# Performance work log

Hardware: AMD Instinct MI355X
Metric: run time of the kernel (lower is better)

## Reference

```python
import jax, jax.numpy as jnp
import numpy as np

N = 100000      # num nodes
E = 1600000     # num edges (avg degree 16)
F_IN = 700      # hardcoded in_feats in build()
H = 128         # args.hidden
EPS = 1e-5      # BatchNorm1d eps


def setup_inputs() -> dict:
    key = jax.random.key(0)
    ks = jax.random.split(key, 12)
    w = lambda k, shape: jax.random.normal(k, shape, dtype=jnp.float32) * 0.05
    return {
        "inputs": jax.random.normal(ks[0], (1, N, F_IN), dtype=jnp.float32),
        "graph": jax.random.randint(ks[1], (1, E, 2), 0, N, dtype=jnp.int32),
        "Wself0": w(ks[2], (F_IN, H)),
        "Wneigh0": w(ks[3], (F_IN, H)),
        "b0": jnp.zeros((H,), jnp.float32),
        "Wself": w(ks[4], (3, H, H)),
        "Wneigh": w(ks[5], (3, H, H)),
        "b": jnp.zeros((3, H), jnp.float32),
        "bn_gamma": jnp.ones((4, H), jnp.float32),
        "bn_beta": jnp.zeros((4, H), jnp.float32),
        "W1": w(ks[6], (H, 64)),
        "b1": jnp.zeros((64,), jnp.float32),
        "bng1": jnp.ones((64,), jnp.float32),
        "bnb1": jnp.zeros((64,), jnp.float32),
        "W2": w(ks[7], (64, 1)),
        "b2": jnp.zeros((1,), jnp.float32),
    }


def _batch_norm(x, g, beta):
    # training-mode BN over node dim (biased variance, as PyTorch normalizes)
    mu = jnp.mean(x, axis=0)
    var = jnp.mean((x - mu) ** 2, axis=0)
    return (x - mu) * jax.lax.rsqrt(var + EPS) * g + beta


def reference(inputs, graph, Wself0, Wneigh0, b0, Wself, Wneigh, b,
              bn_gamma, bn_beta, W1, b1, bng1, bnb1, W2, b2):
    h = inputs[0]                      # [N, F_IN] (squeeze + flatten is a no-op)
    edges = graph[0]                   # [E, 2]
    src, dst = edges[:, 0], edges[:, 1]
    deg = jax.ops.segment_sum(jnp.ones((E,), jnp.float32), dst, num_segments=N)
    denom = jnp.maximum(deg, 1.0)[:, None]   # DGL clamps zero in-degree

    def sage(x, Ws, Wn, bias):
        # SAGEConv(mean): fc before message passing (linearity => equivalent)
        hn = x @ Wn                                                   # [N, H]
        agg = jax.ops.segment_sum(hn[src], dst, num_segments=N) / denom
        return x @ Ws + agg + bias

    # layer 0: no residual
    h = sage(h, Wself0, Wneigh0, b0)
    h = jax.nn.relu(_batch_norm(h, bn_gamma[0], bn_beta[0]))
    # layers 1..3: BN + residual + relu (dropout = identity in eval)
    for l in range(3):
        pre = h
        h = sage(h, Wself[l], Wneigh[l], b[l])
        h = _batch_norm(h, bn_gamma[l + 1], bn_beta[l + 1])
        h = jax.nn.relu(h + pre)

    z = _batch_norm(h @ W1 + b1, bng1, bnb1)
    z = jax.nn.relu(z)
    out = z @ W2 + b2                  # [N, 1]
    return out.T                       # permute(1,0) -> [1, N]
```

## Files before the change

kernel.cpp:

```cpp
#include <hip/hip_runtime.h>
#include <hip/hip_bf16.h>

#define N_NODES 100000
#define N_EDGES 1600000
#define F_IN    700
#define NKB0    22
#define HDIM    128
#define SCAN_B  256
#define NB_SCAN ((N_NODES + SCAN_B - 1) / SCAN_B)

typedef _Float16 half8 __attribute__((ext_vector_type(8)));
typedef _Float16 half4 __attribute__((ext_vector_type(4)));
typedef float floatx4 __attribute__((ext_vector_type(4)));

__device__ __forceinline__ void cp16(const void* g, void* l) {
    __builtin_amdgcn_global_load_lds(
        (const __attribute__((address_space(1))) void*)g,
        (__attribute__((address_space(3))) void*)l, 16, 0, 0);
}

__global__ void count_edges(const int* __restrict__ graph, int* __restrict__ cnt) {
    int e = blockIdx.x * blockDim.x + threadIdx.x;
    if (e < N_EDGES) atomicAdd(&cnt[graph[2 * e + 1]], 1);
}

__global__ void scan1(const int* __restrict__ cnt, int* __restrict__ incl,
                      int* __restrict__ blk) {
    __shared__ int s[SCAN_B];
    int tid = threadIdx.x;
    int i = blockIdx.x * SCAN_B + tid;
    s[tid] = (i < N_NODES) ? cnt[i] : 0;
    __syncthreads();
    for (int off = 1; off < SCAN_B; off <<= 1) {
        int t = (tid >= off) ? s[tid - off] : 0;
        __syncthreads();
        s[tid] += t;
        __syncthreads();
    }
    if (i < N_NODES) incl[i] = s[tid];
    if (tid == SCAN_B - 1) blk[blockIdx.x] = s[tid];
}

__global__ void scan2(const int* __restrict__ blk, int* __restrict__ blkoff) {
    __shared__ int s[512];
    int tid = threadIdx.x;
    s[tid] = (tid < NB_SCAN) ? blk[tid] : 0;
    __syncthreads();
    for (int off = 1; off < 512; off <<= 1) {
        int t = (tid >= off) ? s[tid - off] : 0;
        __syncthreads();
        s[tid] += t;
        __syncthreads();
    }
    if (tid < NB_SCAN) blkoff[tid] = (tid == 0) ? 0 : s[tid - 1];
}

__global__ void scan3(const int* __restrict__ incl, const int* __restrict__ blkoff,
                      int* __restrict__ row_ptr) {
    int i = blockIdx.x * SCAN_B + threadIdx.x;
    if (i < N_NODES) {
        row_ptr[i + 1] = incl[i] + blkoff[i >> 8];
        if (i == 0) row_ptr[0] = 0;
    }
}

__global__ void fill_edges(const int* __restrict__ graph, const int* __restrict__ row_ptr,
                           int* __restrict__ cursor, int* __restrict__ esrc) {
    int e = blockIdx.x * blockDim.x + threadIdx.x;
    if (e < N_EDGES) {
        int src = graph[2 * e];
        int dst = graph[2 * e + 1];
        esrc[row_ptr[dst] + atomicAdd(&cursor[dst], 1)] = src;
    }
}

__global__ void build_wtp0(const float* __restrict__ Wn, const float* __restrict__ Ws,
                           _Float16* __restrict__ out) {
    int q = blockIdx.x * blockDim.x + threadIdx.x;
    if (q >= NKB0 * 256 * 4) return;
    int kb = q >> 10;
    int r  = (q >> 2) & 255;
    int cc = q & 3;
    int k0 = kb * 32 + (cc ^ ((r >> 1) & 3)) * 8;
    half8 v;
    #pragma unroll
    for (int e = 0; e < 8; e++) {
        int k = k0 + e;
        float f = 0.0f;
        if (k < F_IN) f = (r < 128) ? Wn[k * 128 + r] : Ws[k * 128 + (r - 128)];
        v[e] = (_Float16)f;
    }
    *(half8*)&out[(size_t)q * 8] = v;
}

__global__ void build_wtpl(const float* __restrict__ Wn, const float* __restrict__ Ws,
                           _Float16* __restrict__ out) {
    int q = blockIdx.x * blockDim.x + threadIdx.x;
    if (q >= 3 * 4 * 256 * 4) return;
    int l = q >> 12;
    int rem = q & 4095;
    int kb = rem >> 10;
    int r  = (rem >> 2) & 255;
    int cc = rem & 3;
    int k0 = kb * 32 + (cc ^ ((r >> 1) & 3)) * 8;
    half8 v;
    #pragma unroll
    for (int e = 0; e < 8; e++) {
        int k = k0 + e;
        float f = (r < 128) ? Wn[l * 16384 + k * 128 + r]
                            : Ws[l * 16384 + k * 128 + (r - 128)];
        v[e] = (_Float16)f;
    }
    *(half8*)&out[(size_t)q * 8] = v;
}

__global__ __launch_bounds__(256) void gemm0_ns(
    const float* __restrict__ A, int M, int K,
    const _Float16* __restrict__ Wtp, const float* __restrict__ bias,
    const float* __restrict__ zbuf,
    _Float16* __restrict__ Cn, float* __restrict__ Cs) {
    __shared__ char sbuf[2][24576];

    int tid = threadIdx.x;
    int wave = tid >> 6, lane = tid & 63;
    int lm = lane & 15, quad = lane >> 4;
    int wm = wave >> 1, wn = wave & 1;
    int bx = blockIdx.x;
    long row0 = (long)(bx >> 1) * 128;
    int nh = bx & 1;

    floatx4 acc[4][4] = {};

    auto stage = [&](int kb, char* buf) {
        #pragma unroll
        for (int pass = 0; pass < 4; pass++) {
            int q = pass * 256 + tid;
            int r = q >> 3, cc = q & 7;
            int ccg = cc ^ (r & 7);
            long grow = row0 + r;
            if (grow >= M) grow = 0;
            int gk = kb * 32 + ccg * 4;
            const float* src = (gk + 4 <= K) ? (A + grow * (long)K + gk) : zbuf;
            cp16(src, buf + pass * 4096 + wave * 1024);
        }
        const _Float16* wsrc = Wtp + (size_t)kb * 8192 + nh * 4096;
        #pragma unroll
        for (int pass = 0; pass < 2; pass++) {
            cp16(wsrc + (size_t)(pass * 256 + tid) * 8,
                 buf + 16384 + pass * 4096 + wave * 1024);
        }
    };

    stage(0, sbuf[0]);

    for (int kb = 0; kb < NKB0; kb++) {
        int p = kb & 1;
        if (kb + 1 < NKB0) {
            stage(kb + 1, sbuf[p ^ 1]);
            asm volatile("s_waitcnt vmcnt(6)\n\ts_barrier" ::: "memory");
        } else {
            asm volatile("s_waitcnt vmcnt(0)\n\ts_barrier" ::: "memory");
        }

        const float* Af = (const float*)sbuf[p];
        const _Float16* Bf = (const _Float16*)(sbuf[p] + 16384);
        half8 af[4];
        #pragma unroll
        for (int i = 0; i < 4; i++) {
            int row = wm * 64 + i * 16 + lm;
            int c0 = (quad * 2) ^ (row & 7);
            int c1 = (quad * 2 + 1) ^ (row & 7);
            floatx4 f0 = *(const floatx4*)&Af[row * 32 + c0 * 4];
            floatx4 f1 = *(const floatx4*)&Af[row * 32 + c1 * 4];
            af[i][0] = (_Float16)f0[0]; af[i][1] = (_Float16)f0[1];
            af[i][2] = (_Float16)f0[2]; af[i][3] = (_Float16)f0[3];
            af[i][4] = (_Float16)f1[0]; af[i][5] = (_Float16)f1[1];
            af[i][6] = (_Float16)f1[2]; af[i][7] = (_Float16)f1[3];
        }
        #pragma unroll
        for (int j = 0; j < 4; j++) {
            int brow = wn * 64 + j * 16 + lm;
            int ch = quad ^ ((brow >> 1) & 3);
            half8 bf = *(const half8*)&Bf[brow * 32 + ch * 8];
            #pragma unroll
            for (int i = 0; i < 4; i++)
                acc[i][j] = __builtin_amdgcn_mfma_f32_16x16x32_f16(af[i], bf, acc[i][j], 0, 0, 0);
        }
        asm volatile("s_waitcnt lgkmcnt(0)\n\ts_barrier" ::: "memory");
    }

    #pragma unroll
    for (int i = 0; i < 4; i++) {
        long r0 = row0 + wm * 64 + i * 16 + quad * 4;
        #pragma unroll
        for (int j = 0; j < 4; j++) {
            int c = wn * 64 + j * 16 + lm;
            if (nh) {
                float badd = bias[c];
                #pragma unroll
                for (int rr = 0; rr < 4; rr++) {
                    long r = r0 + rr;
                    if (r < M) Cs[r * HDIM + c] = acc[i][j][rr] + badd;
                }
            } else {
                #pragma unroll
                for (int rr = 0; rr < 4; rr++) {
                    long r = r0 + rr;
                    if (r < M) Cn[r * HDIM + c] = (_Float16)acc[i][j][rr];
                }
            }
        }
    }
}

__global__ __launch_bounds__(256) void gemm16_ns(
    const _Float16* __restrict__ A, int M,
    const _Float16* __restrict__ Wtp, const float* __restrict__ bias,
    _Float16* __restrict__ Cn, float* __restrict__ Cs) {
    __shared__ _Float16 sbuf[2][8192];

    int tid = threadIdx.x;
    int wave = tid >> 6, lane = tid & 63;
    int lm = lane & 15, quad = lane >> 4;
    int wm = wave >> 1, wn = wave & 1;
    int bx = blockIdx.x;
    long row0 = (long)(bx >> 1) * 128;
    int nh = bx & 1;

    floatx4 acc[4][4] = {};

    auto stage = [&](int kb, _Float16* buf) {
        #pragma unroll
        for (int pass = 0; pass < 2; pass++) {
            int q = pass * 256 + tid;
            int r = q >> 2, cc = q & 3;
            int ccg = cc ^ ((r >> 1) & 3);
            long grow = row0 + r;
            if (grow >= M) grow = 0;
            cp16(A + grow * (long)HDIM + kb * 32 + ccg * 8,
                 buf + pass * 2048 + wave * 512);
        }
        const _Float16* wsrc = Wtp + (size_t)kb * 8192 + nh * 4096;
        #pragma unroll
        for (int pass = 0; pass < 2; pass++) {
            cp16(wsrc + (size_t)(pass * 256 + tid) * 8,
                 buf + 4096 + pass * 2048 + wave * 512);
        }
    };

    stage(0, sbuf[0]);

    for (int kb = 0; kb < 4; kb++) {
        int p = kb & 1;
        if (kb + 1 < 4) {
            stage(kb + 1, sbuf[p ^ 1]);
            asm volatile("s_waitcnt vmcnt(4)\n\ts_barrier" ::: "memory");
        } else {
            asm volatile("s_waitcnt vmcnt(0)\n\ts_barrier" ::: "memory");
        }

        const _Float16* bp = sbuf[p];
        half8 af[4];
        #pragma unroll
        for (int i = 0; i < 4; i++) {
            int row = wm * 64 + i * 16 + lm;
            int ch = quad ^ ((row >> 1) & 3);
            af[i] = *(const half8*)&bp[row * 32 + ch * 8];
        }
        #pragma unroll
        for (int j = 0; j < 4; j++) {
            int brow = wn * 64 + j * 16 + lm;
            int ch = quad ^ ((brow >> 1) & 3);
            half8 bf = *(const half8*)&bp[4096 + brow * 32 + ch * 8];
            #pragma unroll
            for (int i = 0; i < 4; i++)
                acc[i][j] = __builtin_amdgcn_mfma_f32_16x16x32_f16(af[i], bf, acc[i][j], 0, 0, 0);
        }
        asm volatile("s_waitcnt lgkmcnt(0)\n\ts_barrier" ::: "memory");
    }

    #pragma unroll
    for (int i = 0; i < 4; i++) {
        long r0 = row0 + wm * 64 + i * 16 + quad * 4;
        #pragma unroll
        for (int j = 0; j < 4; j++) {
            int c = wn * 64 + j * 16 + lm;
            if (nh) {
                float badd = bias[c];
                #pragma unroll
                for (int rr = 0; rr < 4; rr++) {
                    long r = r0 + rr;
                    if (r < M) Cs[r * HDIM + c] = acc[i][j][rr] + badd;
                }
            } else {
                #pragma unroll
                for (int rr = 0; rr < 4; rr++) {
                    long r = r0 + rr;
                    if (r < M) Cn[r * HDIM + c] = (_Float16)acc[i][j][rr];
                }
            }
        }
    }
}

__global__ __launch_bounds__(256) void aggregate_w(
    const _Float16* __restrict__ hn, const int* __restrict__ row_ptr,
    const int* __restrict__ esrc, float* __restrict__ pre) {
    int wave = threadIdx.x >> 6, lane = threadIdx.x & 63;
    int n = blockIdx.x * 4 + wave;
    if (n >= N_NODES) return;
    int start = row_ptr[n], end = row_ptr[n + 1];
    int eg = lane >> 4;
    int c8 = (lane & 15) * 8;

    float acc[8] = {};
    for (int base = start; base < end; base += 16) {
        #pragma unroll
        for (int u = 0; u < 4; u++) {
            int e = base + u * 4 + eg;
            if (e < end) {
                int s = esrc[e];
                half8 v = *(const half8*)&hn[(size_t)s * HDIM + c8];
                #pragma unroll
                for (int i = 0; i < 8; i++) acc[i] += (float)v[i];
            }
        }
    }
    #pragma unroll
    for (int i = 0; i < 8; i++) {
        acc[i] += __shfl_xor(acc[i], 16, 64);
        acc[i] += __shfl_xor(acc[i], 32, 64);
    }
    if (eg == 0) {
        float rd = 1.0f / (float)max(end - start, 1);
        size_t off = (size_t)n * HDIM + c8;
        float4 p0 = *(float4*)&pre[off];
        float4 p1 = *(float4*)&pre[off + 4];
        p0.x += acc[0] * rd; p0.y += acc[1] * rd;
        p0.z += acc[2] * rd; p0.w += acc[3] * rd;
        p1.x += acc[4] * rd; p1.y += acc[5] * rd;
        p1.z += acc[6] * rd; p1.w += acc[7] * rd;
        *(float4*)&pre[off]     = p0;
        *(float4*)&pre[off + 4] = p1;
    }
}

__global__ void bn_stats(const float* __restrict__ P, float* __restrict__ gsum,
                         float* __restrict__ gsumsq, int M, int C) {
    int tid = threadIdx.x;
    int c = tid % C;
    int rpb = 256 / C;
    float s = 0.0f, s2 = 0.0f;
    for (int r = blockIdx.x * rpb + tid / C; r < M; r += gridDim.x * rpb) {
        float v = P[(size_t)r * C + c];
        s += v; s2 += v * v;
    }
    __shared__ float ss[256], ss2[256];
    ss[tid] = s; ss2[tid] = s2;
    __syncthreads();
    for (int off = 128; off >= C; off >>= 1) {
        if (tid < off) { ss[tid] += ss[tid + off]; ss2[tid] += ss2[tid + off]; }
        __syncthreads();
    }
    if (tid < C) {
        atomicAdd(&gsum[tid], ss[tid]);
        atomicAdd(&gsumsq[tid], ss2[tid]);
    }
}

__global__ void bn_apply16(const float* __restrict__ P, const _Float16* __restrict__ res16,
                           _Float16* __restrict__ out16,
                           const float* __restrict__ gsum, const float* __restrict__ gsumsq,
                           const float* __restrict__ gamma, const float* __restrict__ beta,
                           int M, int total4, int Cdiv4) {
    __shared__ float ssc[HDIM], ssh[HDIM];
    int tid = threadIdx.x;
    int C = Cdiv4 * 4;
    if (tid < C) {
        float mean = gsum[tid] / (float)M;
        float var = gsumsq[tid] / (float)M - mean * mean;
        float sc = rsqrtf(var + 1e-5f) * gamma[tid];
        ssc[tid] = sc;
        ssh[tid] = beta[tid] - mean * sc;
    }
    __syncthreads();
    for (int f = blockIdx.x * blockDim.x + tid; f < total4;
         f += gridDim.x * blockDim.x) {
        int c4 = (f % Cdiv4) * 4;
        float4 v = ((const float4*)P)[f];
        v.x = v.x * ssc[c4 + 0] + ssh[c4 + 0];
        v.y = v.y * ssc[c4 + 1] + ssh[c4 + 1];
        v.z = v.z * ssc[c4 + 2] + ssh[c4 + 2];
        v.w = v.w * ssc[c4 + 3] + ssh[c4 + 3];
        if (res16) {
            half4 rv = *(const half4*)&res16[(size_t)f * 4];
            v.x += (float)rv[0]; v.y += (float)rv[1];
            v.z += (float)rv[2]; v.w += (float)rv[3];
        }
        half4 h;
        h[0] = (_Float16)fmaxf(v.x, 0.0f); h[1] = (_Float16)fmaxf(v.y, 0.0f);
        h[2] = (_Float16)fmaxf(v.z, 0.0f); h[3] = (_Float16)fmaxf(v.w, 0.0f);
        *(half4*)&out16[(size_t)f * 4] = h;
    }
}

__global__ __launch_bounds__(256) void mlp_gemm(const _Float16* __restrict__ H,
                                                const float* __restrict__ W1,
                                                const float* __restrict__ b1,
                                                float* __restrict__ Z, int M) {
    __shared__ float hs[64 * 132];
    __shared__ float ws[128 * 64];
    int tid = threadIdx.x;
    int tx = tid & 15;
    int ty = tid >> 4;
    int row0 = blockIdx.x * 64;

    #pragma unroll
    for (int t = 0; t < 8; t++) {
        int f = tid + t * 256;
        int r = f >> 4, c4 = (f & 15) * 4;
        *(float4*)&ws[r * 64 + c4] = *(const float4*)&W1[r * 64 + c4];
    }
    #pragma unroll
    for (int t = 0; t < 4; t++) {
        int f = tid + t * 256;
        int r = f >> 4, c8 = (f & 15) * 8;
        int gr = row0 + r;
        if (gr < M) {
            half8 hv = *(const half8*)&H[(size_t)gr * HDIM + c8];
            #pragma unroll
            for (int i = 0; i < 8; i++) hs[r * 132 + c8 + i] = (float)hv[i];
        } else {
            #pragma unroll
            for (int i = 0; i < 8; i++) hs[r * 132 + c8 + i] = 0.0f;
        }
    }
    __syncthreads();

    float acc[4][4] = {};
    for (int k = 0; k < 128; k++) {
        float a[4];
        #pragma unroll
        for (int i = 0; i < 4; i++) a[i] = hs[(ty * 4 + i) * 132 + k];
        float4 b4 = *(const float4*)&ws[k * 64 + tx * 4];
        #pragma unroll
        for (int i = 0; i < 4; i++) {
            acc[i][0] += a[i] * b4.x; acc[i][1] += a[i] * b4.y;
            acc[i][2] += a[i] * b4.z; acc[i][3] += a[i] * b4.w;
        }
    }
    float4 bb = *(const float4*)&b1[tx * 4];
    #pragma unroll
    for (int i = 0; i < 4; i++) {
        int r = row0 + ty * 4 + i;
        if (r < M) {
            float4 v = {acc[i][0] + bb.x, acc[i][1] + bb.y,
                        acc[i][2] + bb.z, acc[i][3] + bb.w};
            *(float4*)&Z[(size_t)r * 64 + tx * 4] = v;
        }
    }
}

__global__ void final_out(const float* __restrict__ Z,
                          const float* __restrict__ gsum, const float* __restrict__ gsumsq,
                          const float* __restrict__ gamma, const float* __restrict__ beta,
                          const float* __restrict__ W2, const float* __restrict__ b2,
                          float* __restrict__ out, int M) {
    __shared__ float ssc[64], ssh[64], sw[64];
    int tid = threadIdx.x;
    if (tid < 64) {
        float mean = gsum[tid] / (float)M;
        float var = gsumsq[tid] / (float)M - mean * mean;
        float sc = rsqrtf(var + 1e-5f) * gamma[tid];
        ssc[tid] = sc;
        ssh[tid] = beta[tid] - mean * sc;
        sw[tid] = W2[tid];
    }
    __syncthreads();
    int n = blockIdx.x * 4 + (tid >> 6);
    int lane = tid & 63;
    if (n >= N_NODES) return;
    float z = Z[(size_t)n * 64 + lane] * ssc[lane] + ssh[lane];
    z = fmaxf(z, 0.0f);
    float v = z * sw[lane];
    #pragma unroll
    for (int off = 32; off >= 1; off >>= 1) v += __shfl_down(v, off, 64);
    if (lane == 0) out[n] = v + b2[0];
}

extern "C" void kernel_launch(void* const* d_in, const int* in_sizes, int n_in,
                              void* d_out, int out_size, void* d_ws, size_t ws_size,
                              hipStream_t stream) {
    const float* X       = (const float*)d_in[0];
    const int*   graph   = (const int*)d_in[1];
    const float* Wself0  = (const float*)d_in[2];
    const float* Wneigh0 = (const float*)d_in[3];
    const float* b0      = (const float*)d_in[4];
    const float* Wself   = (const float*)d_in[5];
    const float* Wneigh  = (const float*)d_in[6];
    const float* bvec    = (const float*)d_in[7];
    const float* bn_g    = (const float*)d_in[8];
    const float* bn_b    = (const float*)d_in[9];
    const float* W1      = (const float*)d_in[10];
    const float* b1      = (const float*)d_in[11];
    const float* bng1    = (const float*)d_in[12];
    const float* bnb1    = (const float*)d_in[13];
    const float* W2      = (const float*)d_in[14];
    const float* b2      = (const float*)d_in[15];
    float* out = (float*)d_out;

    size_t off = 0;
    auto alloc = [&](size_t bytes) {
        void* p = (char*)d_ws + off;
        off += (bytes + 255) & ~(size_t)255;
        return p;
    };
    int* cnt     = (int*)alloc(N_NODES * 4);
    int* cursor  = (int*)alloc(N_NODES * 4);
    int* row_ptr = (int*)alloc((N_NODES + 1) * 4);
    int* incl    = (int*)alloc(N_NODES * 4);
    int* blk     = (int*)alloc(NB_SCAN * 4);
    int* blkoff  = (int*)alloc(NB_SCAN * 4);
    int* esrc    = (int*)alloc((size_t)N_EDGES * 4);
    float*    pre   = (float*)alloc((size_t)N_NODES * HDIM * 4);
    _Float16* h16A  = (_Float16*)alloc((size_t)N_NODES * HDIM * 2);
    _Float16* h16B  = (_Float16*)alloc((size_t)N_NODES * HDIM * 2);
    _Float16* hn16  = (_Float16*)alloc((size_t)N_NODES * HDIM * 2);
    float*    Z     = (float*)alloc((size_t)N_NODES * 64 * 4);
    _Float16* Wtp0  = (_Float16*)alloc((size_t)NKB0 * 8192 * 2);
    _Float16* Wtpl  = (_Float16*)alloc((size_t)3 * 4 * 8192 * 2);
    float*    zbuf  = (float*)alloc(256);
    float* stats = (float*)alloc(256 * 4);
    float* gsum = stats, *gsumsq = stats + 128;

    const int EB = (N_EDGES + 255) / 256;
    const int GB = ((N_NODES + 127) / 128) * 2;
    const int AGB = (N_NODES + 3) / 4;

    hipMemsetAsync(cnt, 0, N_NODES * 4, stream);
    hipMemsetAsync(cursor, 0, N_NODES * 4, stream);
    hipMemsetAsync(zbuf, 0, 256, stream);
    count_edges<<<EB, 256, 0, stream>>>(graph, cnt);
    scan1<<<NB_SCAN, SCAN_B, 0, stream>>>(cnt, incl, blk);
    scan2<<<1, 512, 0, stream>>>(blk, blkoff);
    scan3<<<NB_SCAN, SCAN_B, 0, stream>>>(incl, blkoff, row_ptr);
    fill_edges<<<EB, 256, 0, stream>>>(graph, row_ptr, cursor, esrc);

    build_wtp0<<<(NKB0 * 1024 + 255) / 256, 256, 0, stream>>>(Wneigh0, Wself0, Wtp0);
    build_wtpl<<<(3 * 4096 + 255) / 256, 256, 0, stream>>>(Wneigh, Wself, Wtpl);

    _Float16* hc = h16A;
    _Float16* hx = h16B;

    gemm0_ns<<<GB, 256, 0, stream>>>(X, N_NODES, F_IN, Wtp0, b0, zbuf, hn16, pre);
    aggregate_w<<<AGB, 256, 0, stream>>>(hn16, row_ptr, esrc, pre);
    hipMemsetAsync(stats, 0, 256 * 4, stream);
    bn_stats<<<512, 256, 0, stream>>>(pre, gsum, gsumsq, N_NODES, 128);
    bn_apply16<<<1024, 256, 0, stream>>>(pre, nullptr, hc, gsum, gsumsq,
                                         bn_g, bn_b, N_NODES,
                                         N_NODES * HDIM / 4, HDIM / 4);

    for (int l = 0; l < 3; l++) {
        gemm16_ns<<<GB, 256, 0, stream>>>(hc, N_NODES, Wtpl + (size_t)l * 32768,
                                          bvec + l * HDIM, hn16, pre);
        aggregate_w<<<AGB, 256, 0, stream>>>(hn16, row_ptr, esrc, pre);
        hipMemsetAsync(stats, 0, 256 * 4, stream);
        bn_stats<<<512, 256, 0, stream>>>(pre, gsum, gsumsq, N_NODES, 128);
        bn_apply16<<<1024, 256, 0, stream>>>(pre, hc, hx, gsum, gsumsq,
                                             bn_g + (l + 1) * HDIM,
                                             bn_b + (l + 1) * HDIM, N_NODES,
                                             N_NODES * HDIM / 4, HDIM / 4);
        _Float16* t = hc; hc = hx; hx = t;
    }

    mlp_gemm<<<(N_NODES + 63) / 64, 256, 0, stream>>>(hc, W1, b1, Z, N_NODES);
    hipMemsetAsync(stats, 0, 256 * 4, stream);
    bn_stats<<<512, 256, 0, stream>>>(Z, gsum, gsumsq, N_NODES, 64);
    final_out<<<AGB, 256, 0, stream>>>(Z, gsum, gsumsq, bng1, bnb1, W2, b2,
                                       out, N_NODES);
}
```

Baseline: 1.333 ms.

## Stage layer-0 GEMM A tiles through registers and store fp16 in LDS

The first-layer GEMM no longer copies fp32 input tiles straight from global memory into LDS with global_load_lds. Each thread now loads its A and B fragments into registers two k-blocks ahead, converts A to fp16 once, and writes fp16 tiles into a smaller double-buffered LDS area. This removes the repeated fp32-to-fp16 conversion each wave did on LDS reads and cuts LDS use, which may allow more resident blocks. In exchange it adds register pressure and puts VGPR round-trips and LDS writes into the main loop, where the earlier asynchronous path avoided them.

```diff
diff --git a/kernel.cpp b/kernel.cpp
--- a/kernel.cpp
+++ b/kernel.cpp
@@ -17,6 +17,12 @@
     __builtin_amdgcn_global_load_lds(
         (const __attribute__((address_space(1))) void*)g,
         (__attribute__((address_space(3))) void*)l, 16, 0, 0);
+}
+
+__device__ __forceinline__ floatx4 ld4u(const float* p) {
+    floatx4 v;
+    __builtin_memcpy(&v, p, 16);
+    return v;
 }
 
 __global__ void count_edges(const int* __restrict__ graph, int* __restrict__ cnt) {
@@ -114,12 +120,12 @@
     *(half8*)&out[(size_t)q * 8] = v;
 }
 
-__global__ __launch_bounds__(256) void gemm0_ns(
+__global__ __launch_bounds__(256) void gemm0_rs(
     const float* __restrict__ A, int M, int K,
     const _Float16* __restrict__ Wtp, const float* __restrict__ bias,
     const float* __restrict__ zbuf,
     _Float16* __restrict__ Cn, float* __restrict__ Cs) {
-    __shared__ char sbuf[2][24576];
+    __shared__ _Float16 sbuf[2][8192];
 
     int tid = threadIdx.x;
     int wave = tid >> 6, lane = tid & 63;
@@ -129,64 +135,81 @@
     long row0 = (long)(bx >> 1) * 128;
     int nh = bx & 1;
 
+    int ra1 = tid >> 2, s4 = tid & 3;
+    int ra2 = 64 + ra1;
+    int cc1 = s4 ^ ((ra1 >> 1) & 3);
+    int cc2 = s4 ^ ((ra2 >> 1) & 3);
+    long ga1 = row0 + ra1; if (ga1 >= M) ga1 = 0;
+    long ga2 = row0 + ra2; if (ga2 >= M) ga2 = 0;
+    const float* arow1 = A + ga1 * (long)K;
+    const float* arow2 = A + ga2 * (long)K;
+    const _Float16* wbase = Wtp + nh * 4096;
+
+    floatx4 R[4];
+    half8 Bv[2];
+
+    auto loadA = [&](int kb) {
+        int k1 = kb * 32 + cc1 * 8;
+        int k2 = kb * 32 + cc2 * 8;
+        R[0] = (k1 + 4 <= K) ? ld4u(arow1 + k1)     : ld4u(zbuf);
+        R[1] = (k1 + 8 <= K) ? ld4u(arow1 + k1 + 4) : ld4u(zbuf);
+        R[2] = (k2 + 4 <= K) ? ld4u(arow2 + k2)     : ld4u(zbuf);
+        R[3] = (k2 + 8 <= K) ? ld4u(arow2 + k2 + 4) : ld4u(zbuf);
+    };
+    auto loadB = [&](int kb) {
+        const _Float16* wsrc = wbase + (size_t)kb * 8192;
+        Bv[0] = *(const half8*)(wsrc + tid * 8);
+        Bv[1] = *(const half8*)(wsrc + 2048 + tid * 8);
+    };
+    auto writeAB = [&](_Float16* buf) {
+        half8 h1, h2;
+        #pragma unroll
+        for (int e = 0; e < 4; e++) {
+            h1[e]     = (_Float16)R[0][e];
+            h1[e + 4] = (_Float16)R[1][e];
+            h2[e]     = (_Float16)R[2][e];
+            h2[e + 4] = (_Float16)R[3][e];
+        }
+        *(half8*)&buf[ra1 * 32 + s4 * 8] = h1;
+        *(half8*)&buf[ra2 * 32 + s4 * 8] = h2;
+        *(half8*)&buf[4096 + tid * 8]        = Bv[0];
+        *(half8*)&buf[4096 + 2048 + tid * 8] = Bv[1];
+    };
+
     floatx4 acc[4][4] = {};
 
-    auto stage = [&](int kb, char* buf) {
-        #pragma unroll
-        for (int pass = 0; pass < 4; pass++) {
-            int q = pass * 256 + tid;
-            int r = q >> 3, cc = q & 7;
-            int ccg = cc ^ (r & 7);
-            long grow = row0 + r;
-            if (grow >= M) grow = 0;
-            int gk = kb * 32 + ccg * 4;
-            const float* src = (gk + 4 <= K) ? (A + grow * (long)K + gk) : zbuf;
-            cp16(src, buf + pass * 4096 + wave * 1024);
-        }
-        const _Float16* wsrc = Wtp + (size_t)kb * 8192 + nh * 4096;
-        #pragma unroll
-        for (int pass = 0; pass < 2; pass++) {
-            cp16(wsrc + (size_t)(pass * 256 + tid) * 8,
-                 buf + 16384 + pass * 4096 + wave * 1024);
-        }
-    };
-
-    stage(0, sbuf[0]);
-
+    loadA(0); loadB(0);
+    writeAB(sbuf[0]);
+    loadA(1); loadB(1);
+    asm volatile("s_waitcnt lgkmcnt(0)\n\ts_barrier" ::: "memory");
+
+    #pragma unroll 2
     for (int kb = 0; kb < NKB0; kb++) {
         int p = kb & 1;
-        if (kb + 1 < NKB0) {
-            stage(kb + 1, sbuf[p ^ 1]);
-            asm volatile("s_waitcnt vmcnt(6)\n\ts_barrier" ::: "memory");
-        } else {
-            asm volatile("s_waitcnt vmcnt(0)\n\ts_barrier" ::: "memory");
-        }
-
-        const float* Af = (const float*)sbuf[p];
-        const _Float16* Bf = (const _Float16*)(sbuf[p] + 16384);
+        const _Float16* bp = sbuf[p];
+
         half8 af[4];
         #pragma unroll
         for (int i = 0; i < 4; i++) {
             int row = wm * 64 + i * 16 + lm;
-            int c0 = (quad * 2) ^ (row & 7);
-            int c1 = (quad * 2 + 1) ^ (row & 7);
-            floatx4 f0 = *(const floatx4*)&Af[row * 32 + c0 * 4];
-            floatx4 f1 = *(const floatx4*)&Af[row * 32 + c1 * 4];
-            af[i][0] = (_Float16)f0[0]; af[i][1] = (_Float16)f0[1];
-            af[i][2] = (_Float16)f0[2]; af[i][3] = (_Float16)f0[3];
-            af[i][4] = (_Float16)f1[0]; af[i][5] = (_Float16)f1[1];
-            af[i][6] = (_Float16)f1[2]; af[i][7] = (_Float16)f1[3];
+            int ch = quad ^ ((row >> 1) & 3);
+            af[i] = *(const half8*)&bp[row * 32 + ch * 8];
         }
         #pragma unroll
         for (int j = 0; j < 4; j++) {
             int brow = wn * 64 + j * 16 + lm;
             int ch = quad ^ ((brow >> 1) & 3);
-            half8 bf = *(const half8*)&Bf[brow * 32 + ch * 8];
+            half8 bf = *(const half8*)&bp[4096 + brow * 32 + ch * 8];
             #pragma unroll
             for (int i = 0; i < 4; i++)
                 acc[i][j] = __builtin_amdgcn_mfma_f32_16x16x32_f16(af[i], bf, acc[i][j], 0, 0, 0);
         }
-        asm volatile("s_waitcnt lgkmcnt(0)\n\ts_barrier" ::: "memory");
+
+        if (kb + 1 < NKB0) {
+            writeAB(sbuf[p ^ 1]);
+            if (kb + 2 < NKB0) { loadA(kb + 2); loadB(kb + 2); }
+            asm volatile("s_waitcnt lgkmcnt(0)\n\ts_barrier" ::: "memory");
+        }
     }
 
     #pragma unroll
@@ -552,7 +575,7 @@
     _Float16* hc = h16A;
     _Float16* hx = h16B;
 
-    gemm0_ns<<<GB, 256, 0, stream>>>(X, N_NODES, F_IN, Wtp0, b0, zbuf, hn16, pre);
+    gemm0_rs<<<GB, 256, 0, stream>>>(X, N_NODES, F_IN, Wtp0, b0, zbuf, hn16, pre);
     aggregate_w<<<AGB, 256, 0, stream>>>(hn16, row_ptr, esrc, pre);
     hipMemsetAsync(stats, 0, 256 * 4, stream);
     bn_stats<<<512, 256, 0, stream>>>(pre, gsum, gsumsq, N_NODES, 128);
```

Result: no change. 1.337 ms (+0.3%).

## Fuse BatchNorm statistics into aggregate and MLP kernels with sharded atomics

Applied to the files above, without the earlier changes.

Removes the separate bn_stats kernels by accumulating per-channel sum and sum-of-squares inside aggregate_w and mlp_gemm. Each block first reduces in shared memory, then atomically adds into one of 64 shards to limit atomic contention. The consumers (bn_apply16, final_out) sum the shards before computing mean and variance. This drops one full read pass over the pre-activation and Z buffers per layer, at the cost of a shared-memory reduction, a barrier and extra atomics in the fused kernels.

```diff
diff --git a/kernel.cpp b/kernel.cpp
--- a/kernel.cpp
+++ b/kernel.cpp
@@ -8,6 +8,7 @@
 #define HDIM    128
 #define SCAN_B  256
 #define NB_SCAN ((N_NODES + SCAN_B - 1) / SCAN_B)
+#define NSHARD  64
 
 typedef _Float16 half8 __attribute__((ext_vector_type(8)));
 typedef _Float16 half4 __attribute__((ext_vector_type(4)));
@@ -305,80 +306,87 @@
 
 __global__ __launch_bounds__(256) void aggregate_w(
     const _Float16* __restrict__ hn, const int* __restrict__ row_ptr,
-    const int* __restrict__ esrc, float* __restrict__ pre) {
-    int wave = threadIdx.x >> 6, lane = threadIdx.x & 63;
+    const int* __restrict__ esrc, float* __restrict__ pre,
+    float* __restrict__ stats) {
+    __shared__ float s1[4][HDIM], s2[4][HDIM];
+    int tid = threadIdx.x;
+    int wave = tid >> 6, lane = tid & 63;
     int n = blockIdx.x * 4 + wave;
-    if (n >= N_NODES) return;
-    int start = row_ptr[n], end = row_ptr[n + 1];
+    bool valid = (n < N_NODES);
     int eg = lane >> 4;
     int c8 = (lane & 15) * 8;
 
-    float acc[8] = {};
-    for (int base = start; base < end; base += 16) {
-        #pragma unroll
-        for (int u = 0; u < 4; u++) {
-            int e = base + u * 4 + eg;
-            if (e < end) {
-                int s = esrc[e];
-                half8 v = *(const half8*)&hn[(size_t)s * HDIM + c8];
-                #pragma unroll
-                for (int i = 0; i < 8; i++) acc[i] += (float)v[i];
+    float pv[8] = {};
+    if (valid) {
+        int start = row_ptr[n], end = row_ptr[n + 1];
+        float acc[8] = {};
+        for (int base = start; base < end; base += 16) {
+            #pragma unroll
+            for (int u = 0; u < 4; u++) {
+                int e = base + u * 4 + eg;
+                if (e < end) {
+                    int s = esrc[e];
+                    half8 v = *(const half8*)&hn[(size_t)s * HDIM + c8];
+                    #pragma unroll
+                    for (int i = 0; i < 8; i++) acc[i] += (float)v[i];
+                }
             }
         }
-    }
-    #pragma unroll
-    for (int i = 0; i < 8; i++) {
-        acc[i] += __shfl_xor(acc[i], 16, 64);
-        acc[i] += __shfl_xor(acc[i], 32, 64);
+        #pragma unroll
+        for (int i = 0; i < 8; i++) {
+            acc[i] += __shfl_xor(acc[i], 16, 64);
+            acc[i] += __shfl_xor(acc[i], 32, 64);
+        }
+        if (eg == 0) {
+            float rd = 1.0f / (float)max(end - start, 1);
+            size_t off = (size_t)n * HDIM + c8;
+            float4 p0 = *(float4*)&pre[off];
+            float4 p1 = *(float4*)&pre[off + 4];
+            p0.x += acc[0] * rd; p0.y += acc[1] * rd;
+            p0.z += acc[2] * rd; p0.w += acc[3] * rd;
+            p1.x += acc[4] * rd; p1.y += acc[5] * rd;
+            p1.z += acc[6] * rd; p1.w += acc[7] * rd;
+            *(float4*)&pre[off]     = p0;
+            *(float4*)&pre[off + 4] = p1;
+            pv[0] = p0.x; pv[1] = p0.y; pv[2] = p0.z; pv[3] = p0.w;
+            pv[4] = p1.x; pv[5] = p1.y; pv[6] = p1.z; pv[7] = p1.w;
+        }
     }
     if (eg == 0) {
-        float rd = 1.0f / (float)max(end - start, 1);
-        size_t off = (size_t)n * HDIM + c8;
-        float4 p0 = *(float4*)&pre[off];
-        float4 p1 = *(float4*)&pre[off + 4];
-        p0.x += acc[0] * rd; p0.y += acc[1] * rd;
-        p0.z += acc[2] * rd; p0.w += acc[3] * rd;
-        p1.x += acc[4] * rd; p1.y += acc[5] * rd;
-        p1.z += acc[6] * rd; p1.w += acc[7] * rd;
-        *(float4*)&pre[off]     = p0;
-        *(float4*)&pre[off + 4] = p1;
-    }
-}
-
-__global__ void bn_stats(const float* __restrict__ P, float* __restrict__ gsum,
-                         float* __restrict__ gsumsq, int M, int C) {
-    int tid = threadIdx.x;
-    int c = tid % C;
-    int rpb = 256 / C;
-    float s = 0.0f, s2 = 0.0f;
-    for (int r = blockIdx.x * rpb + tid / C; r < M; r += gridDim.x * rpb) {
-        float v = P[(size_t)r * C + c];
-        s += v; s2 += v * v;
-    }
-    __shared__ float ss[256], ss2[256];
-    ss[tid] = s; ss2[tid] = s2;
+        #pragma unroll
+        for (int i = 0; i < 8; i++) {
+            float v = valid ? pv[i] : 0.0f;
+            s1[wave][c8 + i] = v;
+            s2[wave][c8 + i] = v * v;
+        }
+    }
     __syncthreads();
-    for (int off = 128; off >= C; off >>= 1) {
-        if (tid < off) { ss[tid] += ss[tid + off]; ss2[tid] += ss2[tid + off]; }
-        __syncthreads();
-    }
-    if (tid < C) {
-        atomicAdd(&gsum[tid], ss[tid]);
-        atomicAdd(&gsumsq[tid], ss2[tid]);
+    if (tid < HDIM) {
+        float a = s1[0][tid] + s1[1][tid] + s1[2][tid] + s1[3][tid];
+        float b = s2[0][tid] + s2[1][tid] + s2[2][tid] + s2[3][tid];
+        float* sh = stats + (size_t)(blockIdx.x & (NSHARD - 1)) * 256;
+        atomicAdd(&sh[tid], a);
+        atomicAdd(&sh[128 + tid], b);
     }
 }
 
 __global__ void bn_apply16(const float* __restrict__ P, const _Float16* __restrict__ res16,
                            _Float16* __restrict__ out16,
-                           const float* __restrict__ gsum, const float* __restrict__ gsumsq,
+                           const float* __restrict__ stats,
                            const float* __restrict__ gamma, const float* __restrict__ beta,
                            int M, int total4, int Cdiv4) {
     __shared__ float ssc[HDIM], ssh[HDIM];
     int tid = threadIdx.x;
     int C = Cdiv4 * 4;
     if (tid < C) {
-        float mean = gsum[tid] / (float)M;
-        float var = gsumsq[tid] / (float)M - mean * mean;
+        float s = 0.0f, s2 = 0.0f;
+        #pragma unroll 8
+        for (int k = 0; k < NSHARD; k++) {
+            s  += stats[k * 256 + tid];
+            s2 += stats[k * 256 + 128 + tid];
+        }
+        float mean = s / (float)M;
+        float var = s2 / (float)M - mean * mean;
         float sc = rsqrtf(var + 1e-5f) * gamma[tid];
         ssc[tid] = sc;
         ssh[tid] = beta[tid] - mean * sc;
@@ -407,9 +415,11 @@
 __global__ __launch_bounds__(256) void mlp_gemm(const _Float16* __restrict__ H,
                                                 const float* __restrict__ W1,
                                                 const float* __restrict__ b1,
-                                                float* __restrict__ Z, int M) {
+                                                float* __restrict__ Z,
+                                                float* __restrict__ stats, int M) {
     __shared__ float hs[64 * 132];
     __shared__ float ws[128 * 64];
+    __shared__ float zs1[16][64], zs2[16][64];
     int tid = threadIdx.x;
     int tx = tid & 15;
     int ty = tid >> 4;
@@ -450,27 +460,55 @@
         }
     }
     float4 bb = *(const float4*)&b1[tx * 4];
+    float cs[4] = {}, cq[4] = {};
     #pragma unroll
     for (int i = 0; i < 4; i++) {
         int r = row0 + ty * 4 + i;
         if (r < M) {
-            float4 v = {acc[i][0] + bb.x, acc[i][1] + bb.y,
-                        acc[i][2] + bb.z, acc[i][3] + bb.w};
+            float v0 = acc[i][0] + bb.x;
+            float v1 = acc[i][1] + bb.y;
+            float v2 = acc[i][2] + bb.z;
+            float v3 = acc[i][3] + bb.w;
+            float4 v = {v0, v1, v2, v3};
             *(float4*)&Z[(size_t)r * 64 + tx * 4] = v;
-        }
+            cs[0] += v0; cq[0] += v0 * v0;
+            cs[1] += v1; cq[1] += v1 * v1;
+            cs[2] += v2; cq[2] += v2 * v2;
+            cs[3] += v3; cq[3] += v3 * v3;
+        }
+    }
+    #pragma unroll
+    for (int j = 0; j < 4; j++) {
+        zs1[ty][tx * 4 + j] = cs[j];
+        zs2[ty][tx * 4 + j] = cq[j];
+    }
+    __syncthreads();
+    if (tid < 64) {
+        float a = 0.0f, b = 0.0f;
+        #pragma unroll
+        for (int k = 0; k < 16; k++) { a += zs1[k][tid]; b += zs2[k][tid]; }
+        float* sh = stats + (size_t)(blockIdx.x & (NSHARD - 1)) * 256;
+        atomicAdd(&sh[tid], a);
+        atomicAdd(&sh[128 + tid], b);
     }
 }
 
 __global__ void final_out(const float* __restrict__ Z,
-                          const float* __restrict__ gsum, const float* __restrict__ gsumsq,
+                          const float* __restrict__ stats,
                           const float* __restrict__ gamma, const float* __restrict__ beta,
                           const float* __restrict__ W2, const float* __restrict__ b2,
                           float* __restrict__ out, int M) {
     __shared__ float ssc[64], ssh[64], sw[64];
     int tid = threadIdx.x;
     if (tid < 64) {
-        float mean = gsum[tid] / (float)M;
-        float var = gsumsq[tid] / (float)M - mean * mean;
+        float s = 0.0f, s2 = 0.0f;
+        #pragma unroll 8
+        for (int k = 0; k < NSHARD; k++) {
+            s  += stats[k * 256 + tid];
+            s2 += stats[k * 256 + 128 + tid];
+        }
+        float mean = s / (float)M;
+        float var = s2 / (float)M - mean * mean;
         float sc = rsqrtf(var + 1e-5f) * gamma[tid];
         ssc[tid] = sc;
         ssh[tid] = beta[tid] - mean * sc;
@@ -530,12 +568,12 @@
     _Float16* Wtp0  = (_Float16*)alloc((size_t)NKB0 * 8192 * 2);
     _Float16* Wtpl  = (_Float16*)alloc((size_t)3 * 4 * 8192 * 2);
     float*    zbuf  = (float*)alloc(256);
-    float* stats = (float*)alloc(256 * 4);
-    float* gsum = stats, *gsumsq = stats + 128;
+    float*    stats = (float*)alloc((size_t)NSHARD * 256 * 4);
 
     const int EB = (N_EDGES + 255) / 256;
     const int GB = ((N_NODES + 127) / 128) * 2;
     const int AGB = (N_NODES + 3) / 4;
+    const size_t STB = (size_t)NSHARD * 256 * 4;
 
     hipMemsetAsync(cnt, 0, N_NODES * 4, stream);
     hipMemsetAsync(cursor, 0, N_NODES * 4, stream);
@@ -553,29 +591,26 @@
     _Float16* hx = h16B;
 
     gemm0_ns<<<GB, 256, 0, stream>>>(X, N_NODES, F_IN, Wtp0, b0, zbuf, hn16, pre);
-    aggregate_w<<<AGB, 256, 0, stream>>>(hn16, row_ptr, esrc, pre);
-    hipMemsetAsync(stats, 0, 256 * 4, stream);
-    bn_stats<<<512, 256, 0, stream>>>(pre, gsum, gsumsq, N_NODES, 128);
-    bn_apply16<<<1024, 256, 0, stream>>>(pre, nullptr, hc, gsum, gsumsq,
+    hipMemsetAsync(stats, 0, STB, stream);
+    aggregate_w<<<AGB, 256, 0, stream>>>(hn16, row_ptr, esrc, pre, stats);
+    bn_apply16<<<1024, 256, 0, stream>>>(pre, nullptr, hc, stats,
                                          bn_g, bn_b, N_NODES,
                                          N_NODES * HDIM / 4, HDIM / 4);
 
     for (int l = 0; l < 3; l++) {
         gemm16_ns<<<GB, 256, 0, stream>>>(hc, N_NODES, Wtpl + (size_t)l * 32768,
                                           bvec + l * HDIM, hn16, pre);
-        aggregate_w<<<AGB, 256, 0, stream>>>(hn16, row_ptr, esrc, pre);
-        hipMemsetAsync(stats, 0, 256 * 4, stream);
-        bn_stats<<<512, 256, 0, stream>>>(pre, gsum, gsumsq, N_NODES, 128);
-        bn_apply16<<<1024, 256, 0, stream>>>(pre, hc, hx, gsum, gsumsq,
+        hipMemsetAsync(stats, 0, STB, stream);
+        aggregate_w<<<AGB, 256, 0, stream>>>(hn16, row_ptr, esrc, pre, stats);
+        bn_apply16<<<1024, 256, 0, stream>>>(pre, hc, hx, stats,
                                              bn_g + (l + 1) * HDIM,
                                              bn_b + (l + 1) * HDIM, N_NODES,
                                              N_NODES * HDIM / 4, HDIM / 4);
         _Float16* t = hc; hc = hx; hx = t;
     }
 
-    mlp_gemm<<<(N_NODES + 63) / 64, 256, 0, stream>>>(hc, W1, b1, Z, N_NODES);
-    hipMemsetAsync(stats, 0, 256 * 4, stream);
-    bn_stats<<<512, 256, 0, stream>>>(Z, gsum, gsumsq, N_NODES, 64);
-    final_out<<<AGB, 256, 0, stream>>>(Z, gsum, gsumsq, bng1, bnb1, W2, b2,
+    hipMemsetAsync(stats, 0, STB, stream);
+    mlp_gemm<<<(N_NODES + 63) / 64, 256, 0, stream>>>(hc, W1, b1, Z, stats, N_NODES);
+    final_out<<<AGB, 256, 0, stream>>>(Z, stats, bng1, bnb1, W2, b2,
                                        out, N_NODES);
 }
```

Result: faster. 1.209 ms (-9.3%).
